# Kernel optimization log

Hardware: AMD Instinct MI355X
Metric: run time of the kernel (lower is better)

The kernel has to match this reference:

```python
import jax, jax.numpy as jnp
import numpy as np


def setup_inputs() -> dict:
    key = jax.random.key(0)
    k1, k2 = jax.random.split(key)
    x = jax.random.normal(k1, (8, 256, 64, 64), dtype=jnp.float32)
    # 1x1 conv weight, no bias: [out_c, in_c]
    W = jax.random.normal(k2, (256, 256), dtype=jnp.float32) * (1.0 / np.sqrt(256.0))
    return {"x": x, "W": W}


def reference(x, W):
    b, c, h, w = x.shape
    n = h * w
    xf = x.reshape(b, c, n)  # [b, c, N]
    scale = jnp.asarray(c, x.dtype) ** -0.5
    # sim_map[b, i, j] = sum_c q[b,i,c] * k[b,c,j], q = k = x tokens
    sim = jnp.einsum('bci,bcj->bij', xf, xf) * scale  # [b, N, N]
    attn = jax.nn.softmax(sim, axis=-1)
    # context = attn @ value, then back to [b, c, N]
    ctx = jnp.einsum('bij,bcj->bci', attn, xf)  # [b, c, N]
    ctx = ctx.reshape(b, c, h, w)
    # 1x1 conv, bias-free == channel matmul
    out = jnp.einsum('oc,bchw->bohw', W, ctx)
    return out
```

## Files before the change

kernel.cpp:

```cpp
#include <hip/hip_runtime.h>


typedef __attribute__((ext_vector_type(8))) short short8;
typedef __attribute__((ext_vector_type(4))) float floatx4;
typedef __attribute__((ext_vector_type(16))) float floatx16;
typedef __attribute__((ext_vector_type(4))) int intx4;
typedef __attribute__((ext_vector_type(8))) int intx8;

#define N_TOK 4096
#define C_DIM 256
#define JT 32
#define NT 64

typedef const __attribute__((address_space(1))) unsigned int g_uint;
typedef __attribute__((address_space(3))) unsigned int lds_uint;

__device__ __forceinline__ void gll16(const void* g, void* l) {
  __builtin_amdgcn_global_load_lds((g_uint*)g, (lds_uint*)l, 16, 0, 0);
}

__device__ __forceinline__ unsigned short f2bf(float f) {
  unsigned int u = __builtin_bit_cast(unsigned int, f);
  u += 0x7fffu + ((u >> 16) & 1u);
  return (unsigned short)(u >> 16);
}
__device__ __forceinline__ float bf2f(unsigned short v) {
  return __builtin_bit_cast(float, (unsigned int)v << 16);
}
__device__ __forceinline__ unsigned char f2f8(float f) {
  unsigned u = __builtin_bit_cast(unsigned, f);
  unsigned sgn = (u >> 24) & 0x80u;
  unsigned a = u & 0x7fffffffu;
  if (a > 0x43e40000u) return (unsigned char)(sgn | 0x7e);
  unsigned lsb = (a >> 20) & 1u;
  a += 0x0007ffffu + lsb;
  int e = (int)(a >> 23) - 127;
  if (e < -6) return (unsigned char)sgn;
  if (e > 8) return (unsigned char)(sgn | 0x7e);
  unsigned m = (a >> 20) & 7u;
  return (unsigned char)(sgn | ((unsigned)(e + 7) << 3) | m);
}

__device__ __forceinline__ floatx16 mfma32(short8 a, short8 b, floatx16 c) {
  return __builtin_amdgcn_mfma_f32_32x32x16_bf16(a, b, c, 0, 0, 0);
}
__device__ __forceinline__ floatx4 mfma16(short8 a, short8 b, floatx4 c) {
  return __builtin_amdgcn_mfma_f32_16x16x32_bf16(a, b, c, 0, 0, 0);
}
__device__ __forceinline__ floatx16 mfma_qk(intx8 a, intx8 b, floatx16 c) {
  return __builtin_amdgcn_mfma_scale_f32_32x32x64_f8f6f4(
      a, b, c, 0, 0, 0, 0x7f7f7f7f, 0, 0x7f7f7f7f);
}
__device__ __forceinline__ unsigned cvtpk(float lo, float hi) {
  unsigned d;
  asm("v_cvt_pk_bf16_f32 %0, %1, %2" : "=v"(d) : "v"(lo), "v"(hi));
  return d;
}
__device__ __forceinline__ void swap32(unsigned& a, unsigned& b) {
  asm("v_permlane32_swap_b32 %0, %1" : "+v"(a), "+v"(b));
}

__global__ __launch_bounds__(256) void transpose_conv(
    const float* __restrict__ x, unsigned char* __restrict__ xT8,
    unsigned short* __restrict__ xC) {
  __shared__ float tile[32][33];
  const int b = blockIdx.z;
  const int i0 = blockIdx.x * 32, c0 = blockIdx.y * 32;
  const int tx = threadIdx.x & 31, ty = threadIdx.x >> 5;
  const float* xb = x + (size_t)b * C_DIM * N_TOK;
#pragma unroll
  for (int p = 0; p < 4; ++p) {
    int c = c0 + ty + p * 8;
    float v = xb[(size_t)c * N_TOK + i0 + tx];
    tile[ty + p * 8][tx] = v;
    xC[((size_t)b * C_DIM + c) * N_TOK + i0 + tx] = f2bf(v);
  }
  __syncthreads();
#pragma unroll
  for (int p = 0; p < 4; ++p) {
    int i = i0 + ty + p * 8;
    xT8[((size_t)b * N_TOK + i) * C_DIM + c0 + tx] = f2f8(tile[tx][ty + p * 8]);
  }
}

__global__ __launch_bounds__(256) void wconv(const float* __restrict__ W,
                                             unsigned short* __restrict__ Wb) {
  int idx = blockIdx.x * 256 + threadIdx.x;
  Wb[idx] = f2bf(W[idx]);
}

__global__ __launch_bounds__(256, 2) void attn_kernel(
    const unsigned char* __restrict__ xT8, const unsigned short* __restrict__ xC,
    unsigned short* __restrict__ ctxP, float2* __restrict__ MLd) {
  const int bid = blockIdx.x;
  const int b = bid & 7;
  const int qt = (bid >> 3) & 31;
  const int g = bid >> 8;
  const int tid = threadIdx.x;
  const int lane = tid & 63;
  const int wv = tid >> 6;
  const int l31 = lane & 31;
  const int h = lane >> 5;
  const unsigned char* xT8b = xT8 + (size_t)b * N_TOK * C_DIM;
  const unsigned short* xCb = xC + (size_t)b * N_TOK * C_DIM;
  const char* xT8c = (const char*)xT8b;
  const char* xCc = (const char*)xCb;
  const int qb = qt * 128 + wv * 32;

  __shared__ char lds[2][24576];

  auto STAGE_K = [&](int t, int sel) {
    size_t jb = (size_t)(g * 2048 + t * 32);
    char* Kd = lds[sel] + wv * 1024;
#pragma unroll
    for (int i = 0; i < 2; ++i) {
      int j = i * 16 + wv * 4 + (lane >> 4);
      int c16 = (lane & 15) ^ (j & 15);
      gll16(xT8c + (jb + j) * 256 + c16 * 16, Kd + i * 4096);
    }
  };
  auto STAGE_V = [&](int t, int sel) {
    size_t jb = (size_t)(g * 2048 + t * 32);
    char* Vd = lds[sel] + 8192 + wv * 1024;
#pragma unroll
    for (int i = 0; i < 4; ++i) {
      int r = i * 32 + wv * 8 + (lane >> 3);
      int e = (lane & 7) ^ (r & 7);
      int c = 2 * r + (e >> 2);
      gll16(xCc + (size_t)c * 8192 + jb * 2 + (e & 3) * 16, Vd + i * 4096);
    }
  };

  intx8 q[4];
  {
    const unsigned char* qp = xT8b + (size_t)(qb + l31) * C_DIM + h * 32;
#pragma unroll
    for (int ks = 0; ks < 4; ++ks) {
      intx4 lo = *(const intx4*)(qp + ks * 64);
      intx4 hi = *(const intx4*)(qp + ks * 64 + 16);
      q[ks] = (intx8){lo.x, lo.y, lo.z, lo.w, hi.x, hi.y, hi.z, hi.w};
    }
  }

  floatx16 acc[8];
#pragma unroll
  for (int ct = 0; ct < 8; ++ct)
#pragma unroll
    for (int r = 0; r < 16; ++r) acc[ct][r] = 0.f;
  float m = -1e30f, lsum = 0.f;
  const float SC = 0.09016844005556021f;

  STAGE_K(0, 0);
  STAGE_V(0, 0);

  for (int t = 0; t < NT; ++t) {
    __syncthreads();
    if (t + 1 < NT) {
      STAGE_K(t + 1, (t + 1) & 1);
      STAGE_V(t + 1, (t + 1) & 1);
    }
    const char* Kb = lds[t & 1];
    const char* Vb = lds[t & 1] + 8192;

    floatx16 s;
#pragma unroll
    for (int r = 0; r < 16; ++r) s[r] = 0.f;
    __builtin_amdgcn_s_setprio(1);
#pragma unroll
    for (int ks = 0; ks < 4; ++ks) {
      int ch = ((ks * 4 + h * 2) ^ (l31 & 15)) << 4;
      intx4 ka = *(const intx4*)(Kb + l31 * 256 + ch);
      intx4 kb2 = *(const intx4*)(Kb + l31 * 256 + (ch ^ 16));
      intx8 kf = (intx8){ka.x, ka.y, ka.z, ka.w, kb2.x, kb2.y, kb2.z, kb2.w};
      s = mfma_qk(kf, q[ks], s);
    }
    __builtin_amdgcn_s_setprio(0);

    float mx = s[0];
#pragma unroll
    for (int r = 1; r < 16; ++r) mx = fmaxf(mx, s[r]);
    mx = fmaxf(mx, __shfl_xor(mx, 32));
    float pm = mx * SC;
    bool need = __any(pm > m + 8.0f) != 0;
    float mn = need ? fmaxf(m, pm) : m;
    float al = need ? exp2f(m - mn) : 1.0f;
    m = mn;
    float rsum = 0.f;
#pragma unroll
    for (int r = 0; r < 16; ++r) {
      s[r] = exp2f(s[r] * SC - mn);
      rsum += s[r];
    }
    rsum += __shfl_xor(rsum, 32);
    lsum = lsum * al + rsum;
    if (need) {
#pragma unroll
      for (int r = 0; r < 16; ++r) {
        float ar = __shfl(al, (r & 3) + 8 * (r >> 2) + 4 * h);
#pragma unroll
        for (int ct = 0; ct < 8; ++ct) acc[ct][r] *= ar;
      }
    }

    unsigned pk[8];
#pragma unroll
    for (int pi = 0; pi < 8; ++pi) pk[pi] = cvtpk(s[2 * pi], s[2 * pi + 1]);
    swap32(pk[0], pk[2]); swap32(pk[1], pk[3]);
    swap32(pk[4], pk[6]); swap32(pk[5], pk[7]);
    intx4 a0v = {(int)pk[0], (int)pk[1], (int)pk[2], (int)pk[3]};
    intx4 a1v = {(int)pk[4], (int)pk[5], (int)pk[6], (int)pk[7]};
    short8 pa0 = __builtin_bit_cast(short8, a0v);
    short8 pa1 = __builtin_bit_cast(short8, a1v);

    __builtin_amdgcn_s_setprio(1);
#pragma unroll
    for (int ct = 0; ct < 8; ++ct) {
      int c = ct * 32 + l31;
      int r = c >> 1;
      int pb = (c & 1) << 2;
      int r7 = r & 7;
      short8 v0 = *(const short8*)(Vb + r * 128 + (((h | pb) ^ r7) << 4));
      short8 v1 = *(const short8*)(Vb + r * 128 + ((((2 + h) | pb) ^ r7) << 4));
      acc[ct] = mfma32(pa0, v0, acc[ct]);
      acc[ct] = mfma32(pa1, v1, acc[ct]);
    }
    __builtin_amdgcn_s_setprio(0);
  }

  if (h == 0) {
    float2 ml; ml.x = m; ml.y = lsum;
    MLd[((size_t)g * 8 + b) * N_TOK + qb + l31] = ml;
  }
  unsigned short* cb = ctxP + (((size_t)g * 8 + b) * N_TOK + qb) * C_DIM;
#pragma unroll
  for (int r = 0; r < 16; ++r) {
    int ri = (r & 3) + 8 * (r >> 2) + 4 * h;
#pragma unroll
    for (int ct = 0; ct < 8; ++ct)
      cb[(size_t)ri * C_DIM + ct * 32 + l31] = f2bf(acc[ct][r]);
  }
}

__global__ __launch_bounds__(256) void outgemm(
    const unsigned short* __restrict__ ctxP, const unsigned short* __restrict__ Wb,
    const float2* __restrict__ MLd, float* __restrict__ out) {
  const int bid = blockIdx.x;
  const int b = bid & 7;
  const int it = bid >> 3;
  const int lane = threadIdx.x & 63;
  const int w = threadIdx.x >> 6;
  const int ibase = it * 64 + w * 16;
  const int l15 = lane & 15, lhi = lane >> 4;
  const unsigned short* c0base = ctxP + (size_t)b * N_TOK * C_DIM;
  const unsigned short* c1base = ctxP + (size_t)(8 + b) * N_TOK * C_DIM;
  const float2* ml0b = MLd + (size_t)b * N_TOK;
  const float2* ml1b = MLd + (size_t)(8 + b) * N_TOK;

  const int ia = ibase + l15;
  float2 ma = ml0b[ia], mb = ml1b[ia];
  float Ma = fmaxf(ma.x, mb.x);
  float w0 = exp2f(ma.x - Ma), w1 = exp2f(mb.x - Ma);

  float rden[4];
#pragma unroll
  for (int r = 0; r < 4; ++r) {
    int is = ibase + lhi * 4 + r;
    float2 s0 = ml0b[is], s1 = ml1b[is];
    float Ms = fmaxf(s0.x, s1.x);
    rden[r] = 1.0f / (s0.y * exp2f(s0.x - Ms) + s1.y * exp2f(s1.x - Ms));
  }

  floatx4 acc[16];
#pragma unroll
  for (int i = 0; i < 16; ++i) acc[i] = (floatx4){0.f, 0.f, 0.f, 0.f};

#pragma unroll
  for (int ks = 0; ks < 8; ++ks) {
    short8 o0 = *(const short8*)(c0base + (size_t)ia * C_DIM + ks * 32 + lhi * 8);
    short8 o1 = *(const short8*)(c1base + (size_t)ia * C_DIM + ks * 32 + lhi * 8);
    short8 am;
#pragma unroll
    for (int e = 0; e < 8; ++e)
      am[e] = (short)f2bf(w0 * bf2f((unsigned short)o0[e]) +
                          w1 * bf2f((unsigned short)o1[e]));
#pragma unroll
    for (int ob = 0; ob < 16; ++ob) {
      short8 bw = *(const short8*)(Wb + (size_t)(ob * 16 + l15) * C_DIM + ks * 32 + lhi * 8);
      acc[ob] = mfma16(am, bw, acc[ob]);
    }
  }
  float* outb = out + (size_t)b * C_DIM * N_TOK;
#pragma unroll
  for (int ob = 0; ob < 16; ++ob) {
#pragma unroll
    for (int r = 0; r < 4; ++r) {
      int o = ob * 16 + l15;
      int i = ibase + lhi * 4 + r;
      outb[(size_t)o * N_TOK + i] = acc[ob][r] * rden[r];
    }
  }
}

extern "C" void kernel_launch(void* const* d_in, const int* in_sizes, int n_in,
                              void* d_out, int out_size, void* d_ws, size_t ws_size,
                              hipStream_t stream) {
  const float* x = (const float*)d_in[0];
  const float* W = (const float*)d_in[1];
  float* out = (float*)d_out;
  char* ws = (char*)d_ws;
  const size_t SZ8 = (size_t)8 * N_TOK * C_DIM;
  const size_t SZ = SZ8 * 2;
  unsigned char* xT8 = (unsigned char*)(ws);
  unsigned short* xC = (unsigned short*)(ws + SZ8);
  unsigned short* ctxP = (unsigned short*)(ws + SZ8 + SZ);
  unsigned short* Wb = (unsigned short*)(ws + SZ8 + 3 * SZ);
  float2* MLd = (float2*)(ws + SZ8 + 3 * SZ + C_DIM * C_DIM * 2);

  hipLaunchKernelGGL(transpose_conv, dim3(N_TOK / 32, C_DIM / 32, 8), dim3(256), 0,
                     stream, x, xT8, xC);
  hipLaunchKernelGGL(wconv, dim3((C_DIM * C_DIM) / 256), dim3(256), 0, stream, W, Wb);
  hipLaunchKernelGGL(attn_kernel, dim3(512), dim3(256), 0, stream, xT8, xC, ctxP, MLd);
  hipLaunchKernelGGL(outgemm, dim3(512), dim3(256), 0, stream, ctxP, Wb, MLd, out);
}
```

Baseline: 169.5 us.

## Use FP8 for PV matmul with diagonal residual correction and 64-key tiles

```diff
diff --git a/kernel.cpp b/kernel.cpp
--- a/kernel.cpp
+++ b/kernel.cpp
@@ -9,8 +9,8 @@
 
 #define N_TOK 4096
 #define C_DIM 256
-#define JT 32
-#define NT 64
+#define JT 64
+#define NT 32
 
 typedef const __attribute__((address_space(1))) unsigned int g_uint;
 typedef __attribute__((address_space(3))) unsigned int lds_uint;
@@ -40,29 +40,48 @@
   unsigned m = (a >> 20) & 7u;
   return (unsigned char)(sgn | ((unsigned)(e + 7) << 3) | m);
 }
-
-__device__ __forceinline__ floatx16 mfma32(short8 a, short8 b, floatx16 c) {
-  return __builtin_amdgcn_mfma_f32_32x32x16_bf16(a, b, c, 0, 0, 0);
-}
+__device__ __forceinline__ float f8dec(unsigned b) {
+  unsigned s = (b & 0x80u) << 24;
+  unsigned e = (b >> 3) & 15u;
+  unsigned m = b & 7u;
+  if (e)
+    return __builtin_bit_cast(float, s | ((e + 120u) << 23) | (m << 20));
+  float sub = (float)m * 0.001953125f;
+  return (b & 0x80u) ? -sub : sub;
+}
+
 __device__ __forceinline__ floatx4 mfma16(short8 a, short8 b, floatx4 c) {
   return __builtin_amdgcn_mfma_f32_16x16x32_bf16(a, b, c, 0, 0, 0);
 }
-__device__ __forceinline__ floatx16 mfma_qk(intx8 a, intx8 b, floatx16 c) {
+__device__ __forceinline__ floatx16 mfma8(intx8 a, intx8 b, floatx16 c) {
   return __builtin_amdgcn_mfma_scale_f32_32x32x64_f8f6f4(
       a, b, c, 0, 0, 0, 0x7f7f7f7f, 0, 0x7f7f7f7f);
 }
-__device__ __forceinline__ unsigned cvtpk(float lo, float hi) {
-  unsigned d;
-  asm("v_cvt_pk_bf16_f32 %0, %1, %2" : "=v"(d) : "v"(lo), "v"(hi));
-  return d;
-}
-__device__ __forceinline__ void swap32(unsigned& a, unsigned& b) {
-  asm("v_permlane32_swap_b32 %0, %1" : "+v"(a), "+v"(b));
-}
+template <bool HI>
+__device__ __forceinline__ int pk_fp8(float a, float b, int old) {
+#if __has_builtin(__builtin_amdgcn_cvt_pk_fp8_f32)
+  return __builtin_amdgcn_cvt_pk_fp8_f32(a, b, old, HI);
+#else
+  unsigned w = (unsigned)f2f8(a) | ((unsigned)f2f8(b) << 8);
+  return HI ? (int)(((unsigned)old & 0x0000ffffu) | (w << 16))
+            : (int)(((unsigned)old & 0xffff0000u) | w);
+#endif
+}
+__device__ __forceinline__ float sel4(float a, float b, float c, float d, int k) {
+  float x = (k & 1) ? b : a;
+  float y = (k & 1) ? d : c;
+  return (k & 2) ? y : x;
+}
+__device__ __forceinline__ int sel4i(int a, int b, int c, int d, int k) {
+  int x = (k & 1) ? b : a;
+  int y = (k & 1) ? d : c;
+  return (k & 2) ? y : x;
+}
+
 
 __global__ __launch_bounds__(256) void transpose_conv(
     const float* __restrict__ x, unsigned char* __restrict__ xT8,
-    unsigned short* __restrict__ xC) {
+    unsigned char* __restrict__ xC8p, unsigned short* __restrict__ resid) {
   __shared__ float tile[32][33];
   const int b = blockIdx.z;
   const int i0 = blockIdx.x * 32, c0 = blockIdx.y * 32;
@@ -73,13 +92,19 @@
     int c = c0 + ty + p * 8;
     float v = xb[(size_t)c * N_TOK + i0 + tx];
     tile[ty + p * 8][tx] = v;
-    xC[((size_t)b * C_DIM + c) * N_TOK + i0 + tx] = f2bf(v);
+    int j = i0 + tx, jg = j & 63;
+    int kp = ((jg >> 2) & 1) * 32 + ((jg >> 5) & 1) * 16 + ((jg >> 3) & 3) * 4 + (jg & 3);
+    xC8p[((size_t)b * C_DIM + c) * N_TOK + (j & ~63) + kp] = f2f8(v);
   }
   __syncthreads();
 #pragma unroll
   for (int p = 0; p < 4; ++p) {
     int i = i0 + ty + p * 8;
-    xT8[((size_t)b * N_TOK + i) * C_DIM + c0 + tx] = f2f8(tile[tx][ty + p * 8]);
+    float v = tile[tx][ty + p * 8];
+    unsigned char q8 = f2f8(v);
+    size_t idx = ((size_t)b * N_TOK + i) * C_DIM + c0 + tx;
+    xT8[idx] = q8;
+    resid[idx] = f2bf(v - f8dec(q8));
   }
 }
 
@@ -90,8 +115,8 @@
 }
 
 __global__ __launch_bounds__(256, 2) void attn_kernel(
-    const unsigned char* __restrict__ xT8, const unsigned short* __restrict__ xC,
-    unsigned short* __restrict__ ctxP, float2* __restrict__ MLd) {
+    const unsigned char* __restrict__ xT8, const unsigned char* __restrict__ xC8p,
+    unsigned short* __restrict__ ctxP, float4* __restrict__ MLd) {
   const int bid = blockIdx.x;
   const int b = bid & 7;
   const int qt = (bid >> 3) & 31;
@@ -102,33 +127,34 @@
   const int l31 = lane & 31;
   const int h = lane >> 5;
   const unsigned char* xT8b = xT8 + (size_t)b * N_TOK * C_DIM;
-  const unsigned short* xCb = xC + (size_t)b * N_TOK * C_DIM;
-  const char* xT8c = (const char*)xT8b;
-  const char* xCc = (const char*)xCb;
+  const unsigned char* xCb = xC8p + (size_t)b * C_DIM * N_TOK;
   const int qb = qt * 128 + wv * 32;
 
-  __shared__ char lds[2][24576];
-
+  __shared__ char lds[2][32768];
+
+  const char* kBase;
+  {
+    int j0 = wv * 4 + (lane >> 4);
+    int c16 = (lane & 15) ^ (j0 & 15);
+    kBase = (const char*)xT8b + (size_t)g * 2048 * 256 + j0 * 256 + c16 * 16;
+  }
+  const char* vBase;
+  {
+    int c0 = wv * 16 + (lane >> 2);
+    int kv = (lane & 3) ^ ((lane >> 3) & 3);
+    vBase = (const char*)xCb + (size_t)c0 * N_TOK + g * 2048 + kv * 16;
+  }
   auto STAGE_K = [&](int t, int sel) {
-    size_t jb = (size_t)(g * 2048 + t * 32);
     char* Kd = lds[sel] + wv * 1024;
-#pragma unroll
-    for (int i = 0; i < 2; ++i) {
-      int j = i * 16 + wv * 4 + (lane >> 4);
-      int c16 = (lane & 15) ^ (j & 15);
-      gll16(xT8c + (jb + j) * 256 + c16 * 16, Kd + i * 4096);
-    }
+    const char* src = kBase + (size_t)t * 16384;
+#pragma unroll
+    for (int i = 0; i < 4; ++i) gll16(src + i * 4096, Kd + i * 4096);
   };
   auto STAGE_V = [&](int t, int sel) {
-    size_t jb = (size_t)(g * 2048 + t * 32);
-    char* Vd = lds[sel] + 8192 + wv * 1024;
-#pragma unroll
-    for (int i = 0; i < 4; ++i) {
-      int r = i * 32 + wv * 8 + (lane >> 3);
-      int e = (lane & 7) ^ (r & 7);
-      int c = 2 * r + (e >> 2);
-      gll16(xCc + (size_t)c * 8192 + jb * 2 + (e & 3) * 16, Vd + i * 4096);
-    }
+    char* Vd = lds[sel] + 16384 + wv * 1024;
+    const char* src = vBase + (size_t)t * 64;
+#pragma unroll
+    for (int i = 0; i < 4; ++i) gll16(src + (size_t)i * 64 * N_TOK, Vd + i * 4096);
   };
 
   intx8 q[4];
@@ -141,6 +167,13 @@
       q[ks] = (intx8){lo.x, lo.y, lo.z, lo.w, hi.x, hi.y, hi.z, hi.w};
     }
   }
+
+  const int a0 = l31 * 64 + (((2 * h) ^ ((l31 >> 1) & 3)) << 4);
+
+  const int tdiag = ((qb >> 11) == g) ? ((qb & 2047) >> 6) : -1;
+  const int ud = (qb >> 5) & 1;
+  const int h_o = (l31 >> 2) & 1;
+  float pd_row = 0.f;
 
   floatx16 acc[8];
 #pragma unroll
@@ -160,11 +193,11 @@
       STAGE_V(t + 1, (t + 1) & 1);
     }
     const char* Kb = lds[t & 1];
-    const char* Vb = lds[t & 1] + 8192;
-
-    floatx16 s;
-#pragma unroll
-    for (int r = 0; r < 16; ++r) s[r] = 0.f;
+    const char* Vb = lds[t & 1] + 16384;
+
+    floatx16 s0, s1;
+#pragma unroll
+    for (int r = 0; r < 16; ++r) { s0[r] = 0.f; s1[r] = 0.f; }
     __builtin_amdgcn_s_setprio(1);
 #pragma unroll
     for (int ks = 0; ks < 4; ++ks) {
@@ -172,13 +205,17 @@
       intx4 ka = *(const intx4*)(Kb + l31 * 256 + ch);
       intx4 kb2 = *(const intx4*)(Kb + l31 * 256 + (ch ^ 16));
       intx8 kf = (intx8){ka.x, ka.y, ka.z, ka.w, kb2.x, kb2.y, kb2.z, kb2.w};
-      s = mfma_qk(kf, q[ks], s);
+      s0 = mfma8(kf, q[ks], s0);
+      ka = *(const intx4*)(Kb + (32 + l31) * 256 + ch);
+      kb2 = *(const intx4*)(Kb + (32 + l31) * 256 + (ch ^ 16));
+      kf = (intx8){ka.x, ka.y, ka.z, ka.w, kb2.x, kb2.y, kb2.z, kb2.w};
+      s1 = mfma8(kf, q[ks], s1);
     }
     __builtin_amdgcn_s_setprio(0);
 
-    float mx = s[0];
-#pragma unroll
-    for (int r = 1; r < 16; ++r) mx = fmaxf(mx, s[r]);
+    float mx = fmaxf(s0[0], s1[0]);
+#pragma unroll
+    for (int r = 1; r < 16; ++r) mx = fmaxf(mx, fmaxf(s0[r], s1[r]));
     mx = fmaxf(mx, __shfl_xor(mx, 32));
     float pm = mx * SC;
     bool need = __any(pm > m + 8.0f) != 0;
@@ -188,8 +225,35 @@
     float rsum = 0.f;
 #pragma unroll
     for (int r = 0; r < 16; ++r) {
-      s[r] = exp2f(s[r] * SC - mn);
-      rsum += s[r];
+      s0[r] = exp2f(s0[r] * SC - mn); rsum += s0[r];
+      s1[r] = exp2f(s1[r] * SC - mn); rsum += s1[r];
+    }
+
+    int pk[8];
+#pragma unroll
+    for (int i = 0; i < 4; ++i) {
+      int v = pk_fp8<false>(s0[4 * i], s0[4 * i + 1], 0);
+      pk[i] = pk_fp8<true>(s0[4 * i + 2], s0[4 * i + 3], v);
+      v = pk_fp8<false>(s1[4 * i], s1[4 * i + 1], 0);
+      pk[4 + i] = pk_fp8<true>(s1[4 * i + 2], s1[4 * i + 3], v);
+    }
+
+    if (t == tdiag) {
+      int k1 = l31 & 3, k2 = l31 >> 3;
+      floatx16 sv = ud ? s1 : s0;
+      float aa = sel4(sv[0], sv[1], sv[2], sv[3], k1);
+      float bb = sel4(sv[4], sv[5], sv[6], sv[7], k1);
+      float cc = sel4(sv[8], sv[9], sv[10], sv[11], k1);
+      float dd = sel4(sv[12], sv[13], sv[14], sv[15], k1);
+      float p_d = sel4(aa, bb, cc, dd, k2);
+      int pw = ud ? sel4i(pk[4], pk[5], pk[6], pk[7], k2)
+                  : sel4i(pk[0], pk[1], pk[2], pk[3], k2);
+      float pq = f8dec((unsigned)(pw >> (8 * k1)) & 255u);
+      bool mine = (h == h_o);
+      rsum += mine ? (pq - p_d) : 0.f;
+      float pdl = mine ? pq : 0.f;
+      pdl += __shfl_xor(pdl, 32);
+      pd_row = pdl;
     }
     rsum += __shfl_xor(rsum, 32);
     lsum = lsum * al + rsum;
@@ -202,33 +266,22 @@
       }
     }
 
-    unsigned pk[8];
-#pragma unroll
-    for (int pi = 0; pi < 8; ++pi) pk[pi] = cvtpk(s[2 * pi], s[2 * pi + 1]);
-    swap32(pk[0], pk[2]); swap32(pk[1], pk[3]);
-    swap32(pk[4], pk[6]); swap32(pk[5], pk[7]);
-    intx4 a0v = {(int)pk[0], (int)pk[1], (int)pk[2], (int)pk[3]};
-    intx4 a1v = {(int)pk[4], (int)pk[5], (int)pk[6], (int)pk[7]};
-    short8 pa0 = __builtin_bit_cast(short8, a0v);
-    short8 pa1 = __builtin_bit_cast(short8, a1v);
-
+    intx8 pa = (intx8){pk[0], pk[1], pk[2], pk[3], pk[4], pk[5], pk[6], pk[7]};
     __builtin_amdgcn_s_setprio(1);
 #pragma unroll
     for (int ct = 0; ct < 8; ++ct) {
-      int c = ct * 32 + l31;
-      int r = c >> 1;
-      int pb = (c & 1) << 2;
-      int r7 = r & 7;
-      short8 v0 = *(const short8*)(Vb + r * 128 + (((h | pb) ^ r7) << 4));
-      short8 v1 = *(const short8*)(Vb + r * 128 + ((((2 + h) | pb) ^ r7) << 4));
-      acc[ct] = mfma32(pa0, v0, acc[ct]);
-      acc[ct] = mfma32(pa1, v1, acc[ct]);
+      const char* vp = Vb + ct * 2048;
+      intx4 lo = *(const intx4*)(vp + a0);
+      intx4 hi = *(const intx4*)(vp + (a0 ^ 16));
+      intx8 vf = (intx8){lo.x, lo.y, lo.z, lo.w, hi.x, hi.y, hi.z, hi.w};
+      acc[ct] = mfma8(pa, vf, acc[ct]);
     }
     __builtin_amdgcn_s_setprio(0);
   }
 
   if (h == 0) {
-    float2 ml; ml.x = m; ml.y = lsum;
+    float4 ml;
+    ml.x = m; ml.y = lsum; ml.z = pd_row; ml.w = 0.f;
     MLd[((size_t)g * 8 + b) * N_TOK + qb + l31] = ml;
   }
   unsigned short* cb = ctxP + (((size_t)g * 8 + b) * N_TOK + qb) * C_DIM;
@@ -243,7 +296,8 @@
 
 __global__ __launch_bounds__(256) void outgemm(
     const unsigned short* __restrict__ ctxP, const unsigned short* __restrict__ Wb,
-    const float2* __restrict__ MLd, float* __restrict__ out) {
+    const float4* __restrict__ MLd, const unsigned short* __restrict__ resid,
+    float* __restrict__ out) {
   const int bid = blockIdx.x;
   const int b = bid & 7;
   const int it = bid >> 3;
@@ -253,19 +307,21 @@
   const int l15 = lane & 15, lhi = lane >> 4;
   const unsigned short* c0base = ctxP + (size_t)b * N_TOK * C_DIM;
   const unsigned short* c1base = ctxP + (size_t)(8 + b) * N_TOK * C_DIM;
-  const float2* ml0b = MLd + (size_t)b * N_TOK;
-  const float2* ml1b = MLd + (size_t)(8 + b) * N_TOK;
+  const float4* ml0b = MLd + (size_t)b * N_TOK;
+  const float4* ml1b = MLd + (size_t)(8 + b) * N_TOK;
 
   const int ia = ibase + l15;
-  float2 ma = ml0b[ia], mb = ml1b[ia];
+  float4 ma = ml0b[ia], mb = ml1b[ia];
   float Ma = fmaxf(ma.x, mb.x);
   float w0 = exp2f(ma.x - Ma), w1 = exp2f(mb.x - Ma);
+  float pda = w0 * ma.z + w1 * mb.z;
+  const unsigned short* rrow = resid + (((size_t)b * N_TOK + ia) * C_DIM);
 
   float rden[4];
 #pragma unroll
   for (int r = 0; r < 4; ++r) {
     int is = ibase + lhi * 4 + r;
-    float2 s0 = ml0b[is], s1 = ml1b[is];
+    float4 s0 = ml0b[is], s1 = ml1b[is];
     float Ms = fmaxf(s0.x, s1.x);
     rden[r] = 1.0f / (s0.y * exp2f(s0.x - Ms) + s1.y * exp2f(s1.x - Ms));
   }
@@ -278,11 +334,13 @@
   for (int ks = 0; ks < 8; ++ks) {
     short8 o0 = *(const short8*)(c0base + (size_t)ia * C_DIM + ks * 32 + lhi * 8);
     short8 o1 = *(const short8*)(c1base + (size_t)ia * C_DIM + ks * 32 + lhi * 8);
+    short8 rs = *(const short8*)(rrow + ks * 32 + lhi * 8);
     short8 am;
 #pragma unroll
     for (int e = 0; e < 8; ++e)
       am[e] = (short)f2bf(w0 * bf2f((unsigned short)o0[e]) +
-                          w1 * bf2f((unsigned short)o1[e]));
+                          w1 * bf2f((unsigned short)o1[e]) +
+                          pda * bf2f((unsigned short)rs[e]));
 #pragma unroll
     for (int ob = 0; ob < 16; ++ob) {
       short8 bw = *(const short8*)(Wb + (size_t)(ob * 16 + l15) * C_DIM + ks * 32 + lhi * 8);
@@ -311,14 +369,15 @@
   const size_t SZ8 = (size_t)8 * N_TOK * C_DIM;
   const size_t SZ = SZ8 * 2;
   unsigned char* xT8 = (unsigned char*)(ws);
-  unsigned short* xC = (unsigned short*)(ws + SZ8);
-  unsigned short* ctxP = (unsigned short*)(ws + SZ8 + SZ);
-  unsigned short* Wb = (unsigned short*)(ws + SZ8 + 3 * SZ);
-  float2* MLd = (float2*)(ws + SZ8 + 3 * SZ + C_DIM * C_DIM * 2);
+  unsigned char* xC8p = (unsigned char*)(ws + SZ8);
+  unsigned short* resid = (unsigned short*)(ws + 2 * SZ8);
+  unsigned short* ctxP = (unsigned short*)(ws + 2 * SZ8 + SZ);
+  unsigned short* Wb = (unsigned short*)(ws + 2 * SZ8 + 3 * SZ);
+  float4* MLd = (float4*)(ws + 2 * SZ8 + 3 * SZ + C_DIM * C_DIM * 2);
 
   hipLaunchKernelGGL(transpose_conv, dim3(N_TOK / 32, C_DIM / 32, 8), dim3(256), 0,
-                     stream, x, xT8, xC);
+                     stream, x, xT8, xC8p, resid);
   hipLaunchKernelGGL(wconv, dim3((C_DIM * C_DIM) / 256), dim3(256), 0, stream, W, Wb);
-  hipLaunchKernelGGL(attn_kernel, dim3(512), dim3(256), 0, stream, xT8, xC, ctxP, MLd);
-  hipLaunchKernelGGL(outgemm, dim3(512), dim3(256), 0, stream, ctxP, Wb, MLd, out);
-}
+  hipLaunchKernelGGL(attn_kernel, dim3(512), dim3(256), 0, stream, xT8, xC8p, ctxP, MLd);
+  hipLaunchKernelGGL(outgemm, dim3(512), dim3(256), 0, stream, ctxP, Wb, MLd, resid, out);
+}
```

After: 150.2 us. 1.13x faster.
